# Optimization experiments

Hardware: AMD Instinct MI355X
Metric: run time of the kernel (lower is better)

## Reference

```python
import jax, jax.numpy as jnp
import numpy as np

B, S, HID = 1, 2048, 2048
H, KVH, HD = 16, 8, 128          # query heads, kv heads, head_dim = HID//H
N_REP = H // KVH                 # GQA expansion factor
EPS = 1e-6
THETA = 1e6
SCALING = HD ** (-0.5)           # note: original DIVIDES scores by this (bug kept)


def setup_inputs() -> dict:
    key = jax.random.key(0)
    ks = jax.random.split(key, 5)
    hidden_states = jax.random.normal(ks[0], (B, S, HID), jnp.float32)
    std = 0.02
    wq = jax.random.normal(ks[1], (HID, H * HD), jnp.float32) * std
    wk = jax.random.normal(ks[2], (HID, KVH * HD), jnp.float32) * std
    wv = jax.random.normal(ks[3], (HID, KVH * HD), jnp.float32) * std
    wo = jax.random.normal(ks[4], (H * HD, HID), jnp.float32) * std
    # RoPE tables as in Qwen3: inv_freq over even dims, emb = [freqs, freqs]
    pos = np.arange(S, dtype=np.float64)
    inv_freq = THETA ** (-np.arange(0, HD, 2, dtype=np.float64) / HD)
    freqs = pos[:, None] * inv_freq[None, :]            # [S, HD/2]
    emb = np.concatenate([freqs, freqs], axis=-1)       # [S, HD]
    cos = jnp.asarray(np.cos(emb)[None], jnp.float32)   # [1, S, HD]
    sin = jnp.asarray(np.sin(emb)[None], jnp.float32)
    return {"hidden_states": hidden_states, "cos": cos, "sin": sin,
            "wq": wq, "wk": wk, "wv": wv, "wo": wo}


def _rmsnorm(x):
    # weightless RMSNorm (the module's RMSNorm never applies .weight)
    return x * jax.lax.rsqrt(jnp.mean(x * x, axis=-1, keepdims=True) + EPS)


def _rotate_half(x):
    x1, x2 = jnp.split(x, 2, axis=-1)
    return jnp.concatenate([-x2, x1], axis=-1)


def reference(hidden_states, cos, sin, wq, wk, wv, wo):
    # projections + per-head QK RMSNorm, then [B,H,S,D] layout
    q = _rmsnorm((hidden_states @ wq).reshape(B, S, H, HD)).transpose(0, 2, 1, 3)
    k = _rmsnorm((hidden_states @ wk).reshape(B, S, KVH, HD)).transpose(0, 2, 1, 3)
    v = (hidden_states @ wv).reshape(B, S, KVH, HD).transpose(0, 2, 1, 3)
    # RoPE (cos/sin unsqueezed at head dim)
    c = cos[:, None, :, :]   # [B,1,S,HD]
    s = sin[:, None, :, :]
    q = q * c + _rotate_half(q) * s
    k = k * c + _rotate_half(k) * s
    # GQA repeat_kv: each kv head repeated N_REP consecutive times
    k = jnp.repeat(k, N_REP, axis=1)   # [B,H,S,HD]
    v = jnp.repeat(v, N_REP, axis=1)
    # faithful: scores DIVIDED by head_dim**-0.5 (i.e. * sqrt(HD)); no causal mask
    scores = jnp.einsum('bhqd,bhkd->bhqk', q, k) / SCALING
    probs = jax.nn.softmax(scores, axis=-1)
    attn = jnp.einsum('bhqk,bhkd->bhqd', probs, v)
    out = attn.transpose(0, 2, 1, 3).reshape(B, S, H * HD) @ wo
    return out
```

## Files before the change

### kernel.cpp

```cpp
#include <hip/hip_runtime.h>
#include <hip/hip_bf16.h>
#include <math.h>

#define S 2048
#define HID 2048
#define NH 16
#define KVH 8
#define HD 128
#define EPS 1e-6f
#define QK_SCALE 11.313708498984760390f

typedef __attribute__((ext_vector_type(8))) short s16x8;
typedef __attribute__((ext_vector_type(4))) float f32x4;

__device__ __forceinline__ unsigned short f2bf(float f) {
  __hip_bfloat16 h = __float2bfloat16(f);
  return *(unsigned short*)&h;
}
__device__ __forceinline__ float bf2f(unsigned short u) {
  unsigned int x = ((unsigned int)u) << 16;
  return __builtin_bit_cast(float, x);
}

__device__ __forceinline__ void gload16(const void* g, void* l) {
  __builtin_amdgcn_global_load_lds(
      (const __attribute__((address_space(1))) void*)g,
      (__attribute__((address_space(3))) void*)l, 16, 0, 0);
}

__global__ __launch_bounds__(256) void f32_to_bf16_split(const float* __restrict__ in,
                                                         unsigned short* __restrict__ hi,
                                                         unsigned short* __restrict__ lo,
                                                         int n4) {
  const int i = blockIdx.x * 256 + threadIdx.x;
  if (i < n4) {
    const float4 v = *(const float4*)(in + (size_t)i * 4);
    ushort4 h, l;
    h.x = f2bf(v.x); l.x = f2bf(v.x - bf2f(h.x));
    h.y = f2bf(v.y); l.y = f2bf(v.y - bf2f(h.y));
    h.z = f2bf(v.z); l.z = f2bf(v.z - bf2f(h.z));
    h.w = f2bf(v.w); l.w = f2bf(v.w - bf2f(h.w));
    *(ushort4*)(hi + (size_t)i * 4) = h;
    *(ushort4*)(lo + (size_t)i * 4) = l;
  }
}

__global__ __launch_bounds__(256) void transpose_to_bf16(const float* __restrict__ in,
                                                         unsigned short* __restrict__ out,
                                                         int K, int N) {
  __shared__ float t[64][65];
  const int n0 = blockIdx.x * 64;
  const int k0 = blockIdx.y * 64;
  const int tid = threadIdx.x;

  for (int idx = tid; idx < 64 * 16; idx += 256) {
    const int r = idx >> 4;
    const int c4 = (idx & 15) * 4;
    const float4 v = *(const float4*)(in + (size_t)(k0 + r) * N + n0 + c4);
    t[r][c4 + 0] = v.x; t[r][c4 + 1] = v.y; t[r][c4 + 2] = v.z; t[r][c4 + 3] = v.w;
  }
  __syncthreads();
  for (int idx = tid; idx < 64 * 16; idx += 256) {
    const int a = idx >> 4;
    const int b4 = (idx & 15) * 4;
    ushort4 u;
    u.x = f2bf(t[b4 + 0][a]); u.y = f2bf(t[b4 + 1][a]);
    u.z = f2bf(t[b4 + 2][a]); u.w = f2bf(t[b4 + 3][a]);
    *(ushort4*)(out + (size_t)(n0 + a) * K + k0 + b4) = u;
  }
}

__global__ __launch_bounds__(256) void transpose_to_bf16_split(const float* __restrict__ in,
                                                               unsigned short* __restrict__ ohi,
                                                               unsigned short* __restrict__ olo,
                                                               int K, int N) {
  __shared__ float t[64][65];
  const int n0 = blockIdx.x * 64;
  const int k0 = blockIdx.y * 64;
  const int tid = threadIdx.x;

  for (int idx = tid; idx < 64 * 16; idx += 256) {
    const int r = idx >> 4;
    const int c4 = (idx & 15) * 4;
    const float4 v = *(const float4*)(in + (size_t)(k0 + r) * N + n0 + c4);
    t[r][c4 + 0] = v.x; t[r][c4 + 1] = v.y; t[r][c4 + 2] = v.z; t[r][c4 + 3] = v.w;
  }
  __syncthreads();
  for (int idx = tid; idx < 64 * 16; idx += 256) {
    const int a = idx >> 4;
    const int b4 = (idx & 15) * 4;
    ushort4 h, l;
#pragma unroll
    for (int q = 0; q < 4; ++q) {
      const float v = t[b4 + q][a];
      const unsigned short hu = f2bf(v);
      const unsigned short lu = f2bf(v - bf2f(hu));
      ((unsigned short*)&h)[q] = hu;
      ((unsigned short*)&l)[q] = lu;
    }
    *(ushort4*)(ohi + (size_t)(n0 + a) * K + k0 + b4) = h;
    *(ushort4*)(olo + (size_t)(n0 + a) * K + k0 + b4) = l;
  }
}

#define BK 64

__global__ __launch_bounds__(256) void gemm_qk_fused(const unsigned short* __restrict__ Ahi,
                                                     const unsigned short* __restrict__ Alo,
                                                     const unsigned short* __restrict__ Bhi,
                                                     const unsigned short* __restrict__ Blo,
                                                     const float* __restrict__ cosb,
                                                     const float* __restrict__ sinb,
                                                     unsigned short* __restrict__ qh,
                                                     unsigned short* __restrict__ ql,
                                                     unsigned short* __restrict__ kh,
                                                     unsigned short* __restrict__ kl) {
  __shared__ char smem[49152];
  unsigned short* AsH = (unsigned short*)smem;
  unsigned short* AsL = (unsigned short*)(smem + 8192);
  unsigned short* BsH = (unsigned short*)(smem + 16384);
  unsigned short* BsL = (unsigned short*)(smem + 32768);
  float* Sf = (float*)smem;

  const int tid = threadIdx.x;
  const int lane = tid & 63;
  const int wave = tid >> 6;
  const int hh = blockIdx.x;
  const int m0 = blockIdx.y * 64;
  const int n0 = hh * 128;

  const int qm = (wave >> 1) * 32;
  const int qn = (wave & 1) * 64;
  const int l15 = lane & 15;
  const int quad = lane >> 4;

  const int st_row = lane >> 3;
  const int st_ch = lane & 7;
  const int st_col = ((st_ch ^ st_row) * 8);

  f32x4 acc[2][4] = {};

  for (int k0 = 0; k0 < HID; k0 += BK) {
#pragma unroll
    for (int p = 0; p < 2; ++p) {
      const int rb = wave * 16 + p * 8;
      const size_t aoff = (size_t)(m0 + rb + st_row) * HID + k0 + st_col;
      gload16(Ahi + aoff, &AsH[rb * BK]);
      gload16(Alo + aoff, &AsL[rb * BK]);
    }
#pragma unroll
    for (int p = 0; p < 4; ++p) {
      const int rb = wave * 32 + p * 8;
      const size_t boff = (size_t)(n0 + rb + st_row) * HID + k0 + st_col;
      gload16(Bhi + boff, &BsH[rb * BK]);
      gload16(Blo + boff, &BsL[rb * BK]);
    }
    __syncthreads();

#pragma unroll
    for (int ks = 0; ks < 2; ++ks) {
      s16x8 ah[2], al[2], bh[4], bl[4];
#pragma unroll
      for (int i = 0; i < 2; ++i) {
        const int row = qm + i * 16 + l15;
        const int ro = row * BK + (((ks * 4 + quad) ^ (row & 7)) * 8);
        ah[i] = *(const s16x8*)&AsH[ro];
        al[i] = *(const s16x8*)&AsL[ro];
      }
#pragma unroll
      for (int j = 0; j < 4; ++j) {
        const int row = qn + j * 16 + l15;
        const int ro = row * BK + (((ks * 4 + quad) ^ (row & 7)) * 8);
        bh[j] = *(const s16x8*)&BsH[ro];
        bl[j] = *(const s16x8*)&BsL[ro];
      }
#pragma unroll
      for (int i = 0; i < 2; ++i)
#pragma unroll
        for (int j = 0; j < 4; ++j) {
          acc[i][j] = __builtin_amdgcn_mfma_f32_16x16x32_bf16(ah[i], bh[j], acc[i][j], 0, 0, 0);
          acc[i][j] = __builtin_amdgcn_mfma_f32_16x16x32_bf16(ah[i], bl[j], acc[i][j], 0, 0, 0);
          acc[i][j] = __builtin_amdgcn_mfma_f32_16x16x32_bf16(al[i], bh[j], acc[i][j], 0, 0, 0);
        }
    }
    __syncthreads();
  }

#pragma unroll
  for (int i = 0; i < 2; ++i) {
    const int rbase = qm + i * 16 + quad * 4;
#pragma unroll
    for (int j = 0; j < 4; ++j) {
      const int col = qn + j * 16 + l15;
#pragma unroll
      for (int r = 0; r < 4; ++r)
        Sf[(rbase + r) * 132 + col] = acc[i][j][r];
    }
  }
  __syncthreads();

  const bool is_q = (hh < 16);
  for (int rr = 0; rr < 16; ++rr) {
    const int row = wave * 16 + rr;
    const int s = m0 + row;
    const float x1 = Sf[row * 132 + lane];
    const float x2 = Sf[row * 132 + 64 + lane];

    float ss = x1 * x1 + x2 * x2;
    ss += __shfl_xor(ss, 1);
    ss += __shfl_xor(ss, 2);
    ss += __shfl_xor(ss, 4);
    ss += __shfl_xor(ss, 8);
    ss += __shfl_xor(ss, 16);
    ss += __shfl_xor(ss, 32);
    const float rn = rsqrtf(ss / 128.f + EPS);

    const float c = cosb[(size_t)s * HD + lane];
    const float sn = sinb[(size_t)s * HD + lane];
    float o1 = x1 * rn * c - x2 * rn * sn;
    float o2 = x2 * rn * c + x1 * rn * sn;
    if (is_q) { o1 *= QK_SCALE; o2 *= QK_SCALE; }

    const unsigned short h1 = f2bf(o1), l1 = f2bf(o1 - bf2f(h1));
    const unsigned short h2 = f2bf(o2), l2 = f2bf(o2 - bf2f(h2));
    if (is_q) {
      const size_t base = (size_t)s * 2048 + hh * HD + lane;
      qh[base] = h1; ql[base] = l1;
      qh[base + 64] = h2; ql[base + 64] = l2;
    } else {
      const size_t base = (size_t)s * 1024 + (hh - 16) * HD + lane;
      kh[base] = h1; kl[base] = l1;
      kh[base + 64] = h2; kl[base + 64] = l2;
    }
  }
}

template <int MODE, typename OT>
__global__ __launch_bounds__(256) void gemm_bf16_6464(const unsigned short* __restrict__ A,
                                                      const unsigned short* __restrict__ Bt,
                                                      OT* __restrict__ C,
                                                      int M, int N, int K, int ldc) {
  __shared__ unsigned short As[64 * BK];
  __shared__ unsigned short Bs[64 * BK];

  const int tid = threadIdx.x;
  const int lane = tid & 63;
  const int wave = tid >> 6;
  const int m0 = blockIdx.y * 64;
  const int n0 = blockIdx.x * 64;

  const int qm = (wave >> 1) * 32;
  const int qn = (wave & 1) * 32;
  const int l15 = lane & 15;
  const int quad = lane >> 4;

  const int st_row = lane >> 3;
  const int st_col = (((lane & 7) ^ st_row) * 8);

  f32x4 acc[2][2] = {};

  for (int k0 = 0; k0 < K; k0 += BK) {
#pragma unroll
    for (int p = 0; p < 2; ++p) {
      const int rb = wave * 16 + p * 8;
      gload16(A + (size_t)(m0 + rb + st_row) * K + k0 + st_col, &As[rb * BK]);
      gload16(Bt + (size_t)(n0 + rb + st_row) * K + k0 + st_col, &Bs[rb * BK]);
    }
    __syncthreads();

#pragma unroll
    for (int ks = 0; ks < 2; ++ks) {
      s16x8 a[2], b[2];
#pragma unroll
      for (int i = 0; i < 2; ++i) {
        const int row = qm + i * 16 + l15;
        a[i] = *(const s16x8*)&As[row * BK + (((ks * 4 + quad) ^ (row & 7)) * 8)];
      }
#pragma unroll
      for (int j = 0; j < 2; ++j) {
        const int row = qn + j * 16 + l15;
        b[j] = *(const s16x8*)&Bs[row * BK + (((ks * 4 + quad) ^ (row & 7)) * 8)];
      }
#pragma unroll
      for (int i = 0; i < 2; ++i)
#pragma unroll
        for (int j = 0; j < 2; ++j)
          acc[i][j] = __builtin_amdgcn_mfma_f32_16x16x32_bf16(a[i], b[j], acc[i][j], 0, 0, 0);
    }
    __syncthreads();
  }

#pragma unroll
  for (int i = 0; i < 2; ++i) {
    const int row_base = m0 + qm + i * 16 + quad * 4;
#pragma unroll
    for (int j = 0; j < 2; ++j) {
      const int col = n0 + qn + j * 16 + l15;
      if constexpr (MODE == 0) {
#pragma unroll
        for (int r = 0; r < 4; ++r)
          C[(size_t)(row_base + r) * ldc + col] = acc[i][j][r];
      } else {
        ushort4 u;
        u.x = f2bf(acc[i][j][0]); u.y = f2bf(acc[i][j][1]);
        u.z = f2bf(acc[i][j][2]); u.w = f2bf(acc[i][j][3]);
        *(ushort4*)((unsigned short*)C + (size_t)col * ldc + row_base) = u;
      }
    }
  }
}

#define FA_N 64
#define FA_NT (S / FA_N)

__global__ __launch_bounds__(512, 4) void attn_flash_mfma(const unsigned short* __restrict__ qh,
                                                          const unsigned short* __restrict__ ql,
                                                          const unsigned short* __restrict__ kh,
                                                          const unsigned short* __restrict__ kl,
                                                          const unsigned short* __restrict__ vt,
                                                          unsigned short* __restrict__ out) {
  const int h = blockIdx.y;
  const int kvh = h >> 1;
  const int m0 = blockIdx.x * 64;
  const int tid = threadIdx.x;
  const int lane = tid & 63;
  const int wave = tid >> 6;
  const int rg = wave >> 1;
  const int kg = wave & 1;
  const int l15 = lane & 15;
  const int quad = lane >> 4;

  __shared__ char smem[59392];
  unsigned short* Kh = (unsigned short*)(smem);
  unsigned short* Kl = (unsigned short*)(smem + 16384);
  unsigned short* Vt = (unsigned short*)(smem + 32768);
  unsigned short* Pt = (unsigned short*)(smem + 49152) + wave * 640;

  auto STAGE = [&](int nt) {
#pragma unroll
    for (int p = 0; p < 2; ++p) {
      const int kr = wave * 8 + p * 4 + (lane >> 4);
      const size_t ksrc = (size_t)(nt + kr) * 1024 + kvh * HD + ((lane & 15) ^ (kr & 15)) * 8;
      gload16(kh + ksrc, Kh + (wave * 8 + p * 4) * 128);
      gload16(kl + ksrc, Kl + (wave * 8 + p * 4) * 128);
      const int d = wave * 16 + p * 8 + (lane >> 3);
      const size_t vsrc = (size_t)(kvh * HD + d) * 2048 + nt + ((lane & 7) ^ (d & 7)) * 8;
      gload16(vt + vsrc, Vt + (wave * 16 + p * 8) * 64);
    }
  };

  s16x8 qah[4], qal[4];
  {
    const int qrow = m0 + rg * 16 + l15;
#pragma unroll
    for (int ks = 0; ks < 4; ++ks) {
      const size_t off = (size_t)qrow * 2048 + h * HD + ks * 32 + quad * 8;
      qah[ks] = *(const s16x8*)(qh + off);
      qal[ks] = *(const s16x8*)(ql + off);
    }
  }

  f32x4 O[8] = {};
  float m_i[4], l_i[4];
#pragma unroll
  for (int r = 0; r < 4; ++r) { m_i[r] = -1e30f; l_i[r] = 0.f; }

  for (int t = 0; t < FA_NT; ++t) {
    __syncthreads();
    STAGE(t * FA_N);
    __syncthreads();

    f32x4 sacc[2] = {};
    __builtin_amdgcn_s_setprio(1);
#pragma unroll
    for (int ks = 0; ks < 4; ++ks) {
      s16x8 bh[2], bl[2];
#pragma unroll
      for (int j = 0; j < 2; ++j) {
        const int row = kg * 32 + j * 16 + l15;
        const int ro = row * 128 + (((ks * 4 + quad) ^ l15) * 8);
        bh[j] = *(const s16x8*)&Kh[ro];
        bl[j] = *(const s16x8*)&Kl[ro];
      }
#pragma unroll
      for (int j = 0; j < 2; ++j) {
        sacc[j] = __builtin_amdgcn_mfma_f32_16x16x32_bf16(qah[ks], bh[j], sacc[j], 0, 0, 0);
        sacc[j] = __builtin_amdgcn_mfma_f32_16x16x32_bf16(qah[ks], bl[j], sacc[j], 0, 0, 0);
        sacc[j] = __builtin_amdgcn_mfma_f32_16x16x32_bf16(qal[ks], bh[j], sacc[j], 0, 0, 0);
      }
    }
    __builtin_amdgcn_s_setprio(0);

    float mt[4];
    float dmax = -1e30f;
#pragma unroll
    for (int r = 0; r < 4; ++r) {
      float m = fmaxf(sacc[0][r], sacc[1][r]);
      m = fmaxf(m, __shfl_xor(m, 1));
      m = fmaxf(m, __shfl_xor(m, 2));
      m = fmaxf(m, __shfl_xor(m, 4));
      m = fmaxf(m, __shfl_xor(m, 8));
      mt[r] = m;
      dmax = fmaxf(dmax, m - m_i[r]);
    }
    if (__any(dmax > 8.f)) {
#pragma unroll
      for (int r = 0; r < 4; ++r) {
        const float mnew = fmaxf(m_i[r], mt[r]);
        const float alpha = __expf(m_i[r] - mnew);
        m_i[r] = mnew;
        l_i[r] *= alpha;
#pragma unroll
        for (int jd = 0; jd < 8; ++jd) O[jd][r] *= alpha;
      }
    }
#pragma unroll
    for (int r = 0; r < 4; ++r) {
      const float p0 = __expf(sacc[0][r] - m_i[r]);
      const float p1 = __expf(sacc[1][r] - m_i[r]);
      l_i[r] += p0 + p1;
      const int prow = quad * 4 + r;
      Pt[prow * 40 + l15] = f2bf(p0);
      Pt[prow * 40 + 16 + l15] = f2bf(p1);
    }

    const s16x8 pa = *(const s16x8*)&Pt[l15 * 40 + quad * 8];
    __builtin_amdgcn_s_setprio(1);
#pragma unroll
    for (int jd = 0; jd < 8; ++jd) {
      const int d = jd * 16 + l15;
      const int cp = ((kg * 4 + quad) ^ (d & 7)) * 8;
      const s16x8 vb = *(const s16x8*)&Vt[d * 64 + cp];
      O[jd] = __builtin_amdgcn_mfma_f32_16x16x32_bf16(pa, vb, O[jd], 0, 0, 0);
    }
    __builtin_amdgcn_s_setprio(0);
  }

#pragma unroll
  for (int r = 0; r < 4; ++r) {
    float ls = l_i[r];
    ls += __shfl_xor(ls, 1);
    ls += __shfl_xor(ls, 2);
    ls += __shfl_xor(ls, 4);
    ls += __shfl_xor(ls, 8);
    l_i[r] = ls;
  }

  __syncthreads();
  float* Om = (float*)smem;
  float* ms = (float*)(smem + 32768);
  float* ls2 = (float*)(smem + 33024);

  if (kg == 1) {
#pragma unroll
    for (int r = 0; r < 4; ++r) {
      const int row = rg * 16 + quad * 4 + r;
      if (l15 == 0) { ms[row] = m_i[r]; ls2[row] = l_i[r]; }
#pragma unroll
      for (int jd = 0; jd < 8; ++jd)
        Om[(size_t)row * 128 + jd * 16 + l15] = O[jd][r];
    }
  }
  __syncthreads();
  if (kg == 0) {
#pragma unroll
    for (int r = 0; r < 4; ++r) {
      const int row = rg * 16 + quad * 4 + r;
      const float mB = ms[row];
      const float lB = ls2[row];
      const float mS = fmaxf(m_i[r], mB);
      const float aA = __expf(m_i[r] - mS);
      const float aB = __expf(mB - mS);
      const float inv = 1.f / (aA * l_i[r] + aB * lB);
      const int grow = m0 + row;
#pragma unroll
      for (int jd = 0; jd < 8; ++jd) {
        const float oB = Om[(size_t)row * 128 + jd * 16 + l15];
        out[(size_t)grow * 2048 + h * HD + jd * 16 + l15] =
            f2bf((aA * O[jd][r] + aB * oB) * inv);
      }
    }
  }
}

extern "C" void kernel_launch(void* const* d_in, const int* in_sizes, int n_in,
                              void* d_out, int out_size, void* d_ws, size_t ws_size,
                              hipStream_t stream) {
  const float* hidden = (const float*)d_in[0];
  const float* cosb   = (const float*)d_in[1];
  const float* sinb   = (const float*)d_in[2];
  const float* wq     = (const float*)d_in[3];
  const float* wk     = (const float*)d_in[4];
  const float* wv     = (const float*)d_in[5];
  const float* wo     = (const float*)d_in[6];
  float* out = (float*)d_out;

  char* w = (char*)d_ws;
  unsigned short* q_hi    = (unsigned short*)(w);
  unsigned short* q_lo    = (unsigned short*)(w + (8u << 20));
  unsigned short* k_hi    = (unsigned short*)(w + (16u << 20));
  unsigned short* k_lo    = (unsigned short*)(w + (20u << 20));
  unsigned short* wqkT_hi = (unsigned short*)(w + (24u << 20));
  unsigned short* wqkT_lo = (unsigned short*)(w + (36u << 20));
  unsigned short* hid_hi  = (unsigned short*)(w + (48u << 20));
  unsigned short* hid_lo  = (unsigned short*)(w + (56u << 20));
  unsigned short* vt_b    = (unsigned short*)(w + (64u << 20));
  unsigned short* wvT     = (unsigned short*)(w + (68u << 20));
  unsigned short* woT     = (unsigned short*)(w + (48u << 20));
  unsigned short* a_b     = (unsigned short*)(w + (56u << 20));

  dim3 blk(256);

  f32_to_bf16_split<<<dim3((S * HID / 4 + 255) / 256), blk, 0, stream>>>(hidden, hid_hi, hid_lo, S * HID / 4);
  transpose_to_bf16_split<<<dim3(32, 32), blk, 0, stream>>>(wq, wqkT_hi, wqkT_lo, HID, 2048);
  transpose_to_bf16_split<<<dim3(16, 32), blk, 0, stream>>>(wk, wqkT_hi + (size_t)2048 * 2048,
                                                            wqkT_lo + (size_t)2048 * 2048, HID, 1024);
  transpose_to_bf16<<<dim3(16, 32), blk, 0, stream>>>(wv, wvT, 2048, 1024);

  gemm_qk_fused<<<dim3(24, 32), blk, 0, stream>>>(hid_hi, hid_lo, wqkT_hi, wqkT_lo,
                                                  cosb, sinb, q_hi, q_lo, k_hi, k_lo);

  gemm_bf16_6464<1, unsigned short><<<dim3(1024 / 64, S / 64), blk, 0, stream>>>(
      hid_hi, wvT, vt_b, S, 1024, HID, 2048);

  transpose_to_bf16<<<dim3(32, 32), blk, 0, stream>>>(wo, woT, 2048, HID);

  attn_flash_mfma<<<dim3(S / 64, NH), dim3(512), 0, stream>>>(q_hi, q_lo, k_hi, k_lo, vt_b, a_b);

  gemm_bf16_6464<0, float><<<dim3(HID / 64, S / 64), blk, 0, stream>>>(
      a_b, woT, out, S, HID, 2048, HID);
}
```

Before: 367.1 us.

## Read K tiles directly from global memory and remap blocks to share KV heads

K hi/lo fragments are now loaded straight from global memory into registers instead of being staged through LDS. Only V is staged in shared memory, and the second barrier moves to after the softmax so the V load overlaps the QK^T work. Block indices are remapped so consecutive blocks share the same KV head, which should improve L2 reuse of K and V. The cost is higher global/L2 traffic per wave and exposed global-load latency in the MFMA loop, in exchange for lower LDS use and potentially higher occupancy.

New measurement: 522.7 us. 1.42x slower.

```diff
diff --git a/kernel.cpp b/kernel.cpp
--- a/kernel.cpp
+++ b/kernel.cpp
@@ -319,9 +319,12 @@
                                                           const unsigned short* __restrict__ kl,
                                                           const unsigned short* __restrict__ vt,
                                                           unsigned short* __restrict__ out) {
-  const int h = blockIdx.y;
-  const int kvh = h >> 1;
-  const int m0 = blockIdx.x * 64;
+  const int bid = blockIdx.y * 32 + blockIdx.x;
+  const int kvh = bid & 7;
+  const int jj = bid >> 3;
+  const int h = kvh * 2 + (jj & 1);
+  const int m0 = (jj >> 1) * 64;
+
   const int tid = threadIdx.x;
   const int lane = tid & 63;
   const int wave = tid >> 6;
@@ -330,19 +333,13 @@
   const int l15 = lane & 15;
   const int quad = lane >> 4;
 
-  __shared__ char smem[59392];
-  unsigned short* Kh = (unsigned short*)(smem);
-  unsigned short* Kl = (unsigned short*)(smem + 16384);
-  unsigned short* Vt = (unsigned short*)(smem + 32768);
-  unsigned short* Pt = (unsigned short*)(smem + 49152) + wave * 640;
+  __shared__ char smem[33280];
+  unsigned short* Vt = (unsigned short*)(smem);
+  unsigned short* Pt = (unsigned short*)(smem + 16384) + wave * 640;
 
   auto STAGE = [&](int nt) {
 #pragma unroll
     for (int p = 0; p < 2; ++p) {
-      const int kr = wave * 8 + p * 4 + (lane >> 4);
-      const size_t ksrc = (size_t)(nt + kr) * 1024 + kvh * HD + ((lane & 15) ^ (kr & 15)) * 8;
-      gload16(kh + ksrc, Kh + (wave * 8 + p * 4) * 128);
-      gload16(kl + ksrc, Kl + (wave * 8 + p * 4) * 128);
       const int d = wave * 16 + p * 8 + (lane >> 3);
       const size_t vsrc = (size_t)(kvh * HD + d) * 2048 + nt + ((lane & 7) ^ (d & 7)) * 8;
       gload16(vt + vsrc, Vt + (wave * 16 + p * 8) * 64);
@@ -360,34 +357,38 @@
     }
   }
 
+  const size_t krow_off = (size_t)(kg * 32 + l15) * 1024 + kvh * HD;
+
   f32x4 O[8] = {};
   float m_i[4], l_i[4];
 #pragma unroll
   for (int r = 0; r < 4; ++r) { m_i[r] = -1e30f; l_i[r] = 0.f; }
 
   for (int t = 0; t < FA_NT; ++t) {
+    const int n0 = t * FA_N;
     __syncthreads();
-    STAGE(t * FA_N);
-    __syncthreads();
+    STAGE(n0);
+
+    const unsigned short* kp0 = kh + (size_t)n0 * 1024 + krow_off;
+    const unsigned short* kp1 = kp0 + 16 * 1024;
+    const unsigned short* lp0 = kl + (size_t)n0 * 1024 + krow_off;
+    const unsigned short* lp1 = lp0 + 16 * 1024;
 
     f32x4 sacc[2] = {};
     __builtin_amdgcn_s_setprio(1);
 #pragma unroll
     for (int ks = 0; ks < 4; ++ks) {
-      s16x8 bh[2], bl[2];
-#pragma unroll
-      for (int j = 0; j < 2; ++j) {
-        const int row = kg * 32 + j * 16 + l15;
-        const int ro = row * 128 + (((ks * 4 + quad) ^ l15) * 8);
-        bh[j] = *(const s16x8*)&Kh[ro];
-        bl[j] = *(const s16x8*)&Kl[ro];
-      }
-#pragma unroll
-      for (int j = 0; j < 2; ++j) {
-        sacc[j] = __builtin_amdgcn_mfma_f32_16x16x32_bf16(qah[ks], bh[j], sacc[j], 0, 0, 0);
-        sacc[j] = __builtin_amdgcn_mfma_f32_16x16x32_bf16(qah[ks], bl[j], sacc[j], 0, 0, 0);
-        sacc[j] = __builtin_amdgcn_mfma_f32_16x16x32_bf16(qal[ks], bh[j], sacc[j], 0, 0, 0);
-      }
+      const int co = ks * 32 + quad * 8;
+      const s16x8 bh0 = *(const s16x8*)(kp0 + co);
+      const s16x8 bl0 = *(const s16x8*)(lp0 + co);
+      const s16x8 bh1 = *(const s16x8*)(kp1 + co);
+      const s16x8 bl1 = *(const s16x8*)(lp1 + co);
+      sacc[0] = __builtin_amdgcn_mfma_f32_16x16x32_bf16(qah[ks], bh0, sacc[0], 0, 0, 0);
+      sacc[0] = __builtin_amdgcn_mfma_f32_16x16x32_bf16(qah[ks], bl0, sacc[0], 0, 0, 0);
+      sacc[0] = __builtin_amdgcn_mfma_f32_16x16x32_bf16(qal[ks], bh0, sacc[0], 0, 0, 0);
+      sacc[1] = __builtin_amdgcn_mfma_f32_16x16x32_bf16(qah[ks], bh1, sacc[1], 0, 0, 0);
+      sacc[1] = __builtin_amdgcn_mfma_f32_16x16x32_bf16(qah[ks], bl1, sacc[1], 0, 0, 0);
+      sacc[1] = __builtin_amdgcn_mfma_f32_16x16x32_bf16(qal[ks], bh1, sacc[1], 0, 0, 0);
     }
     __builtin_amdgcn_s_setprio(0);
 
@@ -423,6 +424,8 @@
       Pt[prow * 40 + l15] = f2bf(p0);
       Pt[prow * 40 + 16 + l15] = f2bf(p1);
     }
+
+    __syncthreads();
 
     const s16x8 pa = *(const s16x8*)&Pt[l15 * 40 + quad * 8];
     __builtin_amdgcn_s_setprio(1);
```
